# Kernel tuning notes

Hardware: AMD Instinct MI355X
Metric: run time of the kernel (lower is better)

## Reference

```python
import jax, jax.numpy as jnp
import numpy as np

N = 100000       # nodes
E = 1600000      # edges
DIM_IN = 128
DIM_H = 256
G = 512          # graphs in batch


def setup_inputs() -> dict:
    key = jax.random.key(0)
    ks = jax.random.split(key, 9)
    x = jax.random.normal(ks[0], (N, DIM_IN), dtype=jnp.float32)
    edge_index = jax.random.randint(ks[1], (2, E), 0, N, dtype=jnp.int32)
    batch = jnp.sort(jax.random.randint(ks[2], (N,), 0, G, dtype=jnp.int32))
    # GCNConv weights (glorot-ish scale) + biases, and linear head
    W1 = jax.random.normal(ks[3], (DIM_IN, DIM_H), dtype=jnp.float32) / np.sqrt(DIM_IN)
    b1 = jnp.zeros((DIM_H,), dtype=jnp.float32)
    W2 = jax.random.normal(ks[4], (DIM_H, DIM_H), dtype=jnp.float32) / np.sqrt(DIM_H)
    b2 = jnp.zeros((DIM_H,), dtype=jnp.float32)
    Wl = jax.random.normal(ks[5], (DIM_H, 1), dtype=jnp.float32) / np.sqrt(DIM_H)
    bl = jnp.zeros((1,), dtype=jnp.float32)
    return {"x": x, "edge_index": edge_index, "batch": batch,
            "W1": W1, "b1": b1, "W2": W2, "b2": b2, "Wl": Wl, "bl": bl}


def _gcn_conv(x, W, b, src, dst, norm):
    # PyG GCNConv: h = x @ W; message = norm_e * h[src]; aggregate at dst; + bias
    h = x @ W                                  # [N, d_out]
    msg = h[src] * norm[:, None]               # [E+N, d_out] edge-gathered
    out = jax.ops.segment_sum(msg, dst, num_segments=N)
    return out + b


def reference(x, edge_index, batch, W1, b1, W2, b2, Wl, bl):
    # add self-loops (PyG GCNConv default)
    loops = jnp.arange(N, dtype=edge_index.dtype)
    src = jnp.concatenate([edge_index[0], loops])   # [E+N]
    dst = jnp.concatenate([edge_index[1], loops])   # [E+N]
    # symmetric normalization: deg counted at dst (incl. self-loops)
    deg = jax.ops.segment_sum(jnp.ones_like(src, dtype=x.dtype), dst, num_segments=N)
    dinv = jax.lax.rsqrt(deg)                       # deg >= 1 due to self-loops
    norm = dinv[src] * dinv[dst]                    # [E+N]

    h = jax.nn.relu(_gcn_conv(x, W1, b1, src, dst, norm))
    h = jax.nn.relu(_gcn_conv(h, W2, b2, src, dst, norm))

    # global_mean_pool over graph ids
    sums = jax.ops.segment_sum(h, batch, num_segments=G)                  # [G, d]
    cnts = jax.ops.segment_sum(jnp.ones((N,), h.dtype), batch, num_segments=G)
    pooled = sums / jnp.maximum(cnts, 1.0)[:, None]

    return pooled @ Wl + bl                                              # [G, 1]
```

## Files before the change

kernel.cpp:

```cpp
#include <hip/hip_runtime.h>
#include <hip/hip_fp16.h>
#include <math.h>

typedef _Float16 f16x8 __attribute__((ext_vector_type(8)));
typedef float f32x4 __attribute__((ext_vector_type(4)));


__global__ void k_edge_count(const int* __restrict__ dst, int* __restrict__ ecnt,
                             int* __restrict__ rank, int E) {
    int j = (blockIdx.x * 256 + threadIdx.x) * 2;
    if (j + 1 < E) {
        int2 d = *(const int2*)(dst + j);
        int r0 = atomicAdd(&ecnt[d.x], 1);
        int r1 = atomicAdd(&ecnt[d.y], 1);
        *(int2*)(rank + j) = make_int2(r0, r1);
    } else if (j < E) {
        rank[j] = atomicAdd(&ecnt[dst[j]], 1);
    }
}

__global__ void k_scanA(const int* __restrict__ ecnt, int* __restrict__ bsum, int N) {
    int t = threadIdx.x;
    int base = blockIdx.x * 1024;
    int s = 0;
#pragma unroll
    for (int j = 0; j < 4; ++j) {
        int i = base + j * 256 + t;
        if (i < N) s += ecnt[i];
    }
#pragma unroll
    for (int off = 32; off > 0; off >>= 1) s += __shfl_down(s, off, 64);
    __shared__ int wsum[4];
    if ((t & 63) == 0) wsum[t >> 6] = s;
    __syncthreads();
    if (t == 0) bsum[blockIdx.x] = wsum[0] + wsum[1] + wsum[2] + wsum[3];
}

__global__ void k_scanB(const int* __restrict__ bsum, int* __restrict__ boff, int NB,
                        int* __restrict__ rowstart, int N, int E) {
    __shared__ int sh[256];
    int t = threadIdx.x;
    int v = (t < NB) ? bsum[t] : 0;
    sh[t] = v;
    __syncthreads();
    for (int off = 1; off < 256; off <<= 1) {
        int u = (t >= off) ? sh[t - off] : 0;
        __syncthreads();
        sh[t] += u;
        __syncthreads();
    }
    if (t < NB) boff[t] = sh[t] - v;
    if (t == 0) rowstart[N] = E;
}

__global__ void k_scanC(const int* __restrict__ ecnt, const int* __restrict__ boff,
                        int* __restrict__ rowstart, float* __restrict__ dinv, int N) {
    int t = threadIdx.x;
    int base = blockIdx.x * 1024 + t * 4;
    int e[4];
    int s = 0;
#pragma unroll
    for (int j = 0; j < 4; ++j) {
        int i = base + j;
        e[j] = (i < N) ? ecnt[i] : 0;
        s += e[j];
    }
    __shared__ int sh[256];
    sh[t] = s;
    __syncthreads();
    for (int off = 1; off < 256; off <<= 1) {
        int u = (t >= off) ? sh[t - off] : 0;
        __syncthreads();
        sh[t] += u;
        __syncthreads();
    }
    int off0 = boff[blockIdx.x] + sh[t] - s;
    int run = 0;
#pragma unroll
    for (int j = 0; j < 4; ++j) {
        int i = base + j;
        if (i < N) {
            rowstart[i] = off0 + run;
            dinv[i] = rsqrtf((float)(e[j] + 1));
        }
        run += e[j];
    }
}

__global__ __launch_bounds__(256) void k_scatter8(
    const int* __restrict__ src, const int* __restrict__ dst,
    const int* __restrict__ rowstart, const int* __restrict__ rank,
    int* __restrict__ ssrc, int E, int lo_div) {
    int cls = blockIdx.x & 7;
    int blk = blockIdx.x >> 3;
    int nblk = gridDim.x >> 3;
    int lo = cls * lo_div, hi = lo + lo_div;
    int nchunk = (E + 1023) / 1024;
    for (int ch = blk; ch < nchunk; ch += nblk) {
        int j = ch * 1024 + threadIdx.x * 4;
        if (j + 3 < E) {
            int4 d = *(const int4*)(dst + j);
            int4 s = *(const int4*)(src + j);
            int4 r = *(const int4*)(rank + j);
            if (d.x >= lo && d.x < hi) ssrc[rowstart[d.x] + r.x] = s.x;
            if (d.y >= lo && d.y < hi) ssrc[rowstart[d.y] + r.y] = s.y;
            if (d.z >= lo && d.z < hi) ssrc[rowstart[d.z] + r.z] = s.z;
            if (d.w >= lo && d.w < hi) ssrc[rowstart[d.w] + r.w] = s.w;
        } else {
            for (; j < E; ++j) {
                int dv = dst[j];
                if (dv >= lo && dv < hi) ssrc[rowstart[dv] + rank[j]] = src[j];
            }
        }
    }
}


__global__ __launch_bounds__(256) void k_misc(
    const float* __restrict__ x, __half* __restrict__ xh,
    const float* __restrict__ W1, const float* __restrict__ W2,
    _Float16* __restrict__ W1t, _Float16* __restrict__ W2t,
    const int* __restrict__ batch, int* __restrict__ gstart,
    int* __restrict__ ecnt, int N, int G, int n4) {
    int i = blockIdx.x * 256 + threadIdx.x;
    if (i < n4) {
        float4 v = *(const float4*)(x + (size_t)i * 4);
        union { __half2 h[2]; float2 f; } u;
        u.h[0] = __floats2half2_rn(v.x, v.y);
        u.h[1] = __floats2half2_rn(v.z, v.w);
        *(float2*)(xh + (size_t)i * 4) = u.f;
    }
    if (i < N) {
        ecnt[i] = 0;
        int bi = batch[i];
        int bp = (i == 0) ? -1 : batch[i - 1];
        for (int g = bp + 1; g <= bi; ++g) gstart[g] = i;
        if (i == N - 1) {
            for (int g = bi + 1; g <= G; ++g) gstart[g] = N;
        }
    }
    if (i < 128 * 256) {
        int c = i >> 7, k = i & 127;
        W1t[i] = (_Float16)W1[k * 256 + c];
    } else if (i < 128 * 256 + 256 * 256) {
        int j = i - 128 * 256;
        int c = j >> 8, k = j & 255;
        W2t[j] = (_Float16)W2[k * 256 + c];
    }
}


__global__ __launch_bounds__(256) void k_agg_in(
    const _Float16* __restrict__ xh,
    const int* __restrict__ rowstart, const int* __restrict__ ssrc,
    const float* __restrict__ dinv, _Float16* __restrict__ xa_h, int N) {
    int qw = threadIdx.x >> 4;
    int l = threadIdx.x & 15;
    int v = blockIdx.x * 16 + qw;
    if (v >= N) return;
    float dv = dinv[v];
    float acc[8];
    {
        f16x8 s = *(const f16x8*)(xh + (size_t)v * 128 + l * 8);
#pragma unroll
        for (int j = 0; j < 8; ++j) acc[j] = (float)s[j] * dv;
    }
    int e = rowstart[v], e1 = rowstart[v + 1];
    for (; e + 4 <= e1; e += 4) {
        int u0 = ssrc[e], u1 = ssrc[e + 1], u2 = ssrc[e + 2], u3 = ssrc[e + 3];
        float d0 = dinv[u0], d1 = dinv[u1], d2 = dinv[u2], d3 = dinv[u3];
        f16x8 m0 = *(const f16x8*)(xh + (size_t)u0 * 128 + l * 8);
        f16x8 m1 = *(const f16x8*)(xh + (size_t)u1 * 128 + l * 8);
        f16x8 m2 = *(const f16x8*)(xh + (size_t)u2 * 128 + l * 8);
        f16x8 m3 = *(const f16x8*)(xh + (size_t)u3 * 128 + l * 8);
#pragma unroll
        for (int j = 0; j < 8; ++j) {
            acc[j] = fmaf((float)m0[j], d0, acc[j]);
            acc[j] = fmaf((float)m1[j], d1, acc[j]);
            acc[j] = fmaf((float)m2[j], d2, acc[j]);
            acc[j] = fmaf((float)m3[j], d3, acc[j]);
        }
    }
    for (; e < e1; ++e) {
        int u = ssrc[e];
        float d = dinv[u];
        f16x8 m = *(const f16x8*)(xh + (size_t)u * 128 + l * 8);
#pragma unroll
        for (int j = 0; j < 8; ++j) acc[j] = fmaf((float)m[j], d, acc[j]);
    }
    f16x8 o;
#pragma unroll
    for (int j = 0; j < 8; ++j) o[j] = (_Float16)(acc[j] * dv);
    *(f16x8*)(xa_h + (size_t)v * 128 + l * 8) = o;
}


template<int K, int EPI>
__global__ __launch_bounds__(256, 2) void k_gemm_mfma(
    const _Float16* __restrict__ Ah, const _Float16* __restrict__ Wt,
    const float* __restrict__ dinv, const float* __restrict__ bias,
    _Float16* __restrict__ Ch, int Nrows, int nchunks) {
    constexpr int KS = K / 32;
    constexpr int RB = 2 * K;
    constexpr int NLD = 64 * RB / 4096;
    __shared__ _Float16 As[64 * K];

    int tid = threadIdx.x;
    int l = tid & 63;
    int wv = tid >> 6;

    int bc = wv * 64 + (l & 15);
    int bk = (l >> 4) * 8;
    f16x8 breg[4][KS];
#pragma unroll
    for (int ct = 0; ct < 4; ++ct)
#pragma unroll
        for (int ks = 0; ks < KS; ++ks)
            breg[ct][ks] = *(const f16x8*)(Wt + (size_t)(bc + ct * 16) * K + ks * 32 + bk);
    float bb[4];
    if (EPI == 1) {
#pragma unroll
        for (int ct = 0; ct < 4; ++ct) bb[ct] = bias[bc + ct * 16];
    }

    for (int ch = blockIdx.x; ch < nchunks; ch += gridDim.x) {
        int r0 = ch * 64;
#pragma unroll
        for (int i = 0; i < NLD; ++i) {
            int logical = i * 4096 + tid * 16;
            int row = logical / RB;
            int colb = (logical & (RB - 1)) ^ ((row & 7) << 4);
            int grow = r0 + row;
            grow = grow < Nrows ? grow : Nrows - 1;
            const char* src = (const char*)Ah + (size_t)grow * RB + colb;
            char* dst = (char*)As + i * 4096 + wv * 1024;
            __builtin_amdgcn_global_load_lds(
                (const __attribute__((address_space(1))) void*)src,
                (__attribute__((address_space(3))) void*)dst, 16, 0, 0);
        }
        __syncthreads();

#pragma unroll
        for (int rb = 0; rb < 4; ++rb) {
            f32x4 acc[4];
#pragma unroll
            for (int ct = 0; ct < 4; ++ct) acc[ct] = (f32x4){0.f, 0.f, 0.f, 0.f};
            int row = rb * 16 + (l & 15);
#pragma unroll
            for (int ks = 0; ks < KS; ++ks) {
                int lb = (row * RB + ks * 64 + (l >> 4) * 16) ^ ((l & 7) << 4);
                f16x8 a = *(const f16x8*)((const char*)As + lb);
#pragma unroll
                for (int ct = 0; ct < 4; ++ct)
                    acc[ct] = __builtin_amdgcn_mfma_f32_16x16x32_f16(a, breg[ct][ks], acc[ct], 0, 0, 0);
            }
            int rbase = r0 + rb * 16 + (l >> 4) * 4;
#pragma unroll
            for (int j = 0; j < 4; ++j) {
                int r = rbase + j;
                if (r < Nrows) {
                    if (EPI == 0) {
                        float sc = dinv[r];
#pragma unroll
                        for (int ct = 0; ct < 4; ++ct)
                            Ch[(size_t)r * 256 + bc + ct * 16] = (_Float16)(acc[ct][j] * sc);
                    } else {
#pragma unroll
                        for (int ct = 0; ct < 4; ++ct)
                            Ch[(size_t)r * 256 + bc + ct * 16] =
                                (_Float16)fmaxf(acc[ct][j] + bb[ct], 0.f);
                    }
                }
            }
        }
        __syncthreads();
    }
}


__device__ __forceinline__ void acc_h4s(float4& acc, float2 raw) {
    union { float2 f; __half2 h[2]; } u;
    u.f = raw;
    float2 p0 = __half22float2(u.h[0]);
    float2 p1 = __half22float2(u.h[1]);
    acc.x += p0.x; acc.y += p0.y; acc.z += p1.x; acc.w += p1.y;
}

__global__ __launch_bounds__(256) void k_aggregate(
    const __half* __restrict__ hsh, const int* __restrict__ rowstart,
    const int* __restrict__ ssrc, const float* __restrict__ dinv,
    const float* __restrict__ bias, __half* __restrict__ h2h, int N) {
    int w = threadIdx.x >> 6;
    int l = threadIdx.x & 63;
    int v = blockIdx.x * 4 + w;
    if (v >= N) return;
    float4 acc = make_float4(0.f, 0.f, 0.f, 0.f);
    acc_h4s(acc, *(const float2*)(hsh + (size_t)v * 256 + l * 4));
    int e = rowstart[v], e1 = rowstart[v + 1];
    for (; e + 4 <= e1; e += 4) {
        int u0 = ssrc[e], u1 = ssrc[e + 1], u2 = ssrc[e + 2], u3 = ssrc[e + 3];
        float2 m0 = *(const float2*)(hsh + (size_t)u0 * 256 + l * 4);
        float2 m1 = *(const float2*)(hsh + (size_t)u1 * 256 + l * 4);
        float2 m2 = *(const float2*)(hsh + (size_t)u2 * 256 + l * 4);
        float2 m3 = *(const float2*)(hsh + (size_t)u3 * 256 + l * 4);
        acc_h4s(acc, m0);
        acc_h4s(acc, m1);
        acc_h4s(acc, m2);
        acc_h4s(acc, m3);
    }
    for (; e < e1; ++e) {
        int u = ssrc[e];
        acc_h4s(acc, *(const float2*)(hsh + (size_t)u * 256 + l * 4));
    }
    float d = dinv[v];
    float4 b = *(const float4*)(bias + l * 4);
    union { __half2 h[2]; float2 f; } uo;
    uo.h[0] = __floats2half2_rn(fmaxf(fmaf(acc.x, d, b.x), 0.f),
                                fmaxf(fmaf(acc.y, d, b.y), 0.f));
    uo.h[1] = __floats2half2_rn(fmaxf(fmaf(acc.z, d, b.z), 0.f),
                                fmaxf(fmaf(acc.w, d, b.w), 0.f));
    *(float2*)(h2h + (size_t)v * 256 + l * 4) = uo.f;
}


__global__ __launch_bounds__(256) void k_poolhead(
    const __half* __restrict__ h2h, const int* __restrict__ gstart,
    const float* __restrict__ Wl, const float* __restrict__ bl,
    float* __restrict__ out, int G) {
    int g = blockIdx.x;
    int t = threadIdx.x;
    int i0 = gstart[g], i1 = gstart[g + 1];
    float s = 0.f;
    for (int i = i0; i < i1; ++i) s += __half2float(h2h[(size_t)i * 256 + t]);
    float pooled = s / fmaxf((float)(i1 - i0), 1.f);
    float v = pooled * Wl[t];
#pragma unroll
    for (int off = 32; off > 0; off >>= 1) v += __shfl_down(v, off, 64);
    __shared__ float red[4];
    if ((t & 63) == 0) red[t >> 6] = v;
    __syncthreads();
    if (t == 0) out[g] = red[0] + red[1] + red[2] + red[3] + bl[0];
}


extern "C" void kernel_launch(void* const* d_in, const int* in_sizes, int n_in,
                              void* d_out, int out_size, void* d_ws, size_t ws_size,
                              hipStream_t stream) {
    const float* x  = (const float*)d_in[0];
    const int* ei   = (const int*)d_in[1];
    const int* batch= (const int*)d_in[2];
    const float* W1 = (const float*)d_in[3];
    const float* b1 = (const float*)d_in[4];
    const float* W2 = (const float*)d_in[5];
    const float* b2 = (const float*)d_in[6];
    const float* Wl = (const float*)d_in[7];
    const float* bl = (const float*)d_in[8];
    float* out = (float*)d_out;

    const int N = in_sizes[2];
    const int E = in_sizes[1] / 2;
    const int G = out_size;

    char* wsp = (char*)d_ws;
    size_t off = 0;
    auto carve = [&](size_t bytes) -> void* {
        void* p = wsp + off;
        off = (off + bytes + 255) & ~(size_t)255;
        return p;
    };
    float* bufA    = (float*)carve((size_t)N * 256 * 4);
    float* bufB    = (float*)carve((size_t)N * 256 * 4);
    float* dinv    = (float*)carve((size_t)N * 4);
    int* ecnt      = (int*)carve((size_t)N * 4);
    int* rowstart  = (int*)carve((size_t)(N + 1) * 4);
    int* rank      = (int*)carve((size_t)E * 4);
    int* ssrc      = (int*)carve((size_t)E * 4);
    const int NB = (N + 1023) / 1024;
    int* bsum      = (int*)carve((size_t)NB * 4);
    int* boff      = (int*)carve((size_t)NB * 4);
    int* gstart    = (int*)carve((size_t)(G + 1) * 4);
    _Float16* W1t  = (_Float16*)carve((size_t)256 * 128 * 2);
    _Float16* W2t  = (_Float16*)carve((size_t)256 * 256 * 2);
    (void)ws_size;

    _Float16* xh   = (_Float16*)bufA;
    _Float16* xa_h = (_Float16*)((char*)bufA + (size_t)N * 128 * 2);
    _Float16* h1h  = (_Float16*)((char*)bufA + (size_t)N * 128 * 4);
    _Float16* hsh  = (_Float16*)bufB;
    __half*   h2h  = (__half*)((char*)bufB + (size_t)N * 256 * 2);

    const int* esrc = ei;
    const int* edst = ei + E;

    int nchunks = (N + 63) / 64;
    int n4 = N * 32;
    int lo_div = (N + 7) / 8;

    hipLaunchKernelGGL(k_misc, dim3((n4 + 255) / 256), dim3(256), 0, stream,
                       x, (__half*)xh, W1, W2, W1t, W2t, batch, gstart, ecnt, N, G, n4);
    hipLaunchKernelGGL(k_edge_count, dim3((E / 2 + 255) / 256), dim3(256), 0, stream,
                       edst, ecnt, rank, E);
    hipLaunchKernelGGL(k_scanA, dim3(NB), dim3(256), 0, stream, ecnt, bsum, N);
    hipLaunchKernelGGL(k_scanB, dim3(1), dim3(256), 0, stream, bsum, boff, NB, rowstart, N, E);
    hipLaunchKernelGGL(k_scanC, dim3(NB), dim3(256), 0, stream, ecnt, boff, rowstart, dinv, N);
    hipLaunchKernelGGL(k_scatter8, dim3(2048), dim3(256), 0, stream,
                       esrc, edst, rowstart, rank, ssrc, E, lo_div);

    hipLaunchKernelGGL(k_agg_in, dim3((N + 15) / 16), dim3(256), 0, stream,
                       xh, rowstart, ssrc, dinv, xa_h, N);
    hipLaunchKernelGGL((k_gemm_mfma<128, 1>), dim3(512), dim3(256), 0, stream,
                       xa_h, W1t, (const float*)nullptr, b1, h1h, N, nchunks);
    hipLaunchKernelGGL((k_gemm_mfma<256, 0>), dim3(512), dim3(256), 0, stream,
                       h1h, W2t, dinv, (const float*)nullptr, hsh, N, nchunks);
    hipLaunchKernelGGL(k_aggregate, dim3((N + 3) / 4), dim3(256), 0, stream,
                       (const __half*)hsh, rowstart, ssrc, dinv, b2, h2h, N);
    hipLaunchKernelGGL(k_poolhead, dim3(G), dim3(256), 0, stream,
                       h2h, gstart, Wl, bl, out, G);
}
```

Baseline: 423.3 us.

## Fuse layer-1 and layer-2 GEMMs through shared-memory intermediate tile

```diff
diff --git a/kernel.cpp b/kernel.cpp
--- a/kernel.cpp
+++ b/kernel.cpp
@@ -195,15 +195,15 @@
 }
 
 
-template<int K, int EPI>
-__global__ __launch_bounds__(256, 2) void k_gemm_mfma(
-    const _Float16* __restrict__ Ah, const _Float16* __restrict__ Wt,
-    const float* __restrict__ dinv, const float* __restrict__ bias,
-    _Float16* __restrict__ Ch, int Nrows, int nchunks) {
-    constexpr int KS = K / 32;
-    constexpr int RB = 2 * K;
-    constexpr int NLD = 64 * RB / 4096;
-    __shared__ _Float16 As[64 * K];
+__global__ __launch_bounds__(256, 2) void k_gemm12(
+    const _Float16* __restrict__ Ah, const _Float16* __restrict__ W1t,
+    const _Float16* __restrict__ W2t, const float* __restrict__ bias1,
+    const float* __restrict__ dinv, _Float16* __restrict__ hsh,
+    int Nrows, int nchunks) {
+    constexpr int K1 = 128, KS1 = K1 / 32, RB1 = 2 * K1;
+    constexpr int K2 = 256, KS2 = K2 / 32, RB2 = 2 * K2;
+    __shared__ _Float16 As[64 * K1];
+    __shared__ _Float16 Hs[64 * K2];
 
     int tid = threadIdx.x;
     int l = tid & 63;
@@ -211,28 +211,32 @@
 
     int bc = wv * 64 + (l & 15);
     int bk = (l >> 4) * 8;
-    f16x8 breg[4][KS];
+    f16x8 breg1[4][KS1];
 #pragma unroll
     for (int ct = 0; ct < 4; ++ct)
 #pragma unroll
-        for (int ks = 0; ks < KS; ++ks)
-            breg[ct][ks] = *(const f16x8*)(Wt + (size_t)(bc + ct * 16) * K + ks * 32 + bk);
-    float bb[4];
-    if (EPI == 1) {
-#pragma unroll
-        for (int ct = 0; ct < 4; ++ct) bb[ct] = bias[bc + ct * 16];
-    }
+        for (int ks = 0; ks < KS1; ++ks)
+            breg1[ct][ks] = *(const f16x8*)(W1t + (size_t)(bc + ct * 16) * K1 + ks * 32 + bk);
+    f16x8 breg2[4][KS2];
+#pragma unroll
+    for (int ct = 0; ct < 4; ++ct)
+#pragma unroll
+        for (int ks = 0; ks < KS2; ++ks)
+            breg2[ct][ks] = *(const f16x8*)(W2t + (size_t)(bc + ct * 16) * K2 + ks * 32 + bk);
+    float bb1[4];
+#pragma unroll
+    for (int ct = 0; ct < 4; ++ct) bb1[ct] = bias1[bc + ct * 16];
 
     for (int ch = blockIdx.x; ch < nchunks; ch += gridDim.x) {
         int r0 = ch * 64;
 #pragma unroll
-        for (int i = 0; i < NLD; ++i) {
+        for (int i = 0; i < 4; ++i) {
             int logical = i * 4096 + tid * 16;
-            int row = logical / RB;
-            int colb = (logical & (RB - 1)) ^ ((row & 7) << 4);
+            int row = logical >> 8;
+            int colb = (logical & (RB1 - 1)) ^ ((row & 7) << 4);
             int grow = r0 + row;
             grow = grow < Nrows ? grow : Nrows - 1;
-            const char* src = (const char*)Ah + (size_t)grow * RB + colb;
+            const char* src = (const char*)Ah + (size_t)grow * RB1 + colb;
             char* dst = (char*)As + i * 4096 + wv * 1024;
             __builtin_amdgcn_global_load_lds(
                 (const __attribute__((address_space(1))) void*)src,
@@ -247,29 +251,50 @@
             for (int ct = 0; ct < 4; ++ct) acc[ct] = (f32x4){0.f, 0.f, 0.f, 0.f};
             int row = rb * 16 + (l & 15);
 #pragma unroll
-            for (int ks = 0; ks < KS; ++ks) {
-                int lb = (row * RB + ks * 64 + (l >> 4) * 16) ^ ((l & 7) << 4);
+            for (int ks = 0; ks < KS1; ++ks) {
+                int lb = (row * RB1 + ks * 64 + (l >> 4) * 16) ^ ((l & 7) << 4);
                 f16x8 a = *(const f16x8*)((const char*)As + lb);
 #pragma unroll
                 for (int ct = 0; ct < 4; ++ct)
-                    acc[ct] = __builtin_amdgcn_mfma_f32_16x16x32_f16(a, breg[ct][ks], acc[ct], 0, 0, 0);
+                    acc[ct] = __builtin_amdgcn_mfma_f32_16x16x32_f16(a, breg1[ct][ks], acc[ct], 0, 0, 0);
+            }
+            int rloc = rb * 16 + (l >> 4) * 4;
+#pragma unroll
+            for (int j = 0; j < 4; ++j) {
+                int rl = rloc + j;
+#pragma unroll
+                for (int ct = 0; ct < 4; ++ct) {
+                    float v = fmaxf(acc[ct][j] + bb1[ct], 0.f);
+                    int boff = rl * RB2 + (((bc + ct * 16) * 2) ^ ((rl & 7) << 4));
+                    *(_Float16*)((char*)Hs + boff) = (_Float16)v;
+                }
+            }
+        }
+        __syncthreads();
+
+#pragma unroll
+        for (int rb = 0; rb < 4; ++rb) {
+            f32x4 acc[4];
+#pragma unroll
+            for (int ct = 0; ct < 4; ++ct) acc[ct] = (f32x4){0.f, 0.f, 0.f, 0.f};
+            int row = rb * 16 + (l & 15);
+#pragma unroll
+            for (int ks = 0; ks < KS2; ++ks) {
+                int lb = (row * RB2 + ks * 64 + (l >> 4) * 16) ^ ((l & 7) << 4);
+                f16x8 a = *(const f16x8*)((const char*)Hs + lb);
+#pragma unroll
+                for (int ct = 0; ct < 4; ++ct)
+                    acc[ct] = __builtin_amdgcn_mfma_f32_16x16x32_f16(a, breg2[ct][ks], acc[ct], 0, 0, 0);
             }
             int rbase = r0 + rb * 16 + (l >> 4) * 4;
 #pragma unroll
             for (int j = 0; j < 4; ++j) {
                 int r = rbase + j;
                 if (r < Nrows) {
-                    if (EPI == 0) {
-                        float sc = dinv[r];
-#pragma unroll
-                        for (int ct = 0; ct < 4; ++ct)
-                            Ch[(size_t)r * 256 + bc + ct * 16] = (_Float16)(acc[ct][j] * sc);
-                    } else {
-#pragma unroll
-                        for (int ct = 0; ct < 4; ++ct)
-                            Ch[(size_t)r * 256 + bc + ct * 16] =
-                                (_Float16)fmaxf(acc[ct][j] + bb[ct], 0.f);
-                    }
+                    float sc = dinv[r];
+#pragma unroll
+                    for (int ct = 0; ct < 4; ++ct)
+                        hsh[(size_t)r * 256 + bc + ct * 16] = (_Float16)(acc[ct][j] * sc);
                 }
             }
         }
@@ -385,7 +410,6 @@
 
     _Float16* xh   = (_Float16*)bufA;
     _Float16* xa_h = (_Float16*)((char*)bufA + (size_t)N * 128 * 2);
-    _Float16* h1h  = (_Float16*)((char*)bufA + (size_t)N * 128 * 4);
     _Float16* hsh  = (_Float16*)bufB;
     __half*   h2h  = (__half*)((char*)bufB + (size_t)N * 256 * 2);
 
@@ -408,10 +432,8 @@
 
     hipLaunchKernelGGL(k_agg_in, dim3((N + 15) / 16), dim3(256), 0, stream,
                        xh, rowstart, ssrc, dinv, xa_h, N);
-    hipLaunchKernelGGL((k_gemm_mfma<128, 1>), dim3(512), dim3(256), 0, stream,
-                       xa_h, W1t, (const float*)nullptr, b1, h1h, N, nchunks);
-    hipLaunchKernelGGL((k_gemm_mfma<256, 0>), dim3(512), dim3(256), 0, stream,
-                       h1h, W2t, dinv, (const float*)nullptr, hsh, N, nchunks);
+    hipLaunchKernelGGL(k_gemm12, dim3(512), dim3(256), 0, stream,
+                       xa_h, W1t, W2t, b1, dinv, hsh, N, nchunks);
     hipLaunchKernelGGL(k_aggregate, dim3((N + 3) / 4), dim3(256), 0, stream,
                        (const __half*)hsh, rowstart, ssrc, dinv, b2, h2h, N);
     hipLaunchKernelGGL(k_poolhead, dim3(G), dim3(256), 0, stream,
```

New measurement: 482.8 us. +14.1%, slower.
